# Optimization experiments

Hardware: AMD Instinct MI355X
Metric: run time of the kernel (lower is better)

Reference implementation:

```python
import jax, jax.numpy as jnp
import numpy as np

N_ANCHORS = 10647
N_CLASSES = 80
N_OUT = 5 + N_CLASSES
N_GT = 2048
POS_IOU = 0.7
NEG_IOU = 0.3
N_SAMPLE = 256
POS_RATIO = 0.5


def _cxcy_to_corners(b):
    return jnp.concatenate([b[:, :2] - b[:, 2:4] / 2, b[:, :2] + b[:, 2:4] / 2], axis=-1)


def _iou(a, b):
    # a: [N,4] corner boxes, b: [M,4] corner boxes -> [N,M]
    lt = jnp.maximum(a[:, None, :2], b[None, :, :2])
    rb = jnp.minimum(a[:, None, 2:], b[None, :, 2:])
    wh = jnp.clip(rb - lt, 0.0)
    inter = wh[..., 0] * wh[..., 1]
    area_a = (a[:, 2] - a[:, 0]) * (a[:, 3] - a[:, 1])
    area_b = (b[:, 2] - b[:, 0]) * (b[:, 3] - b[:, 1])
    return inter / (area_a[:, None] + area_b[None, :] - inter)


def _bce_logits(x, t):
    # numerically stable BCEWithLogits, elementwise
    return jnp.maximum(x, 0.0) - x * t + jnp.log1p(jnp.exp(-jnp.abs(x)))


def _demote_first(labels, value, excess):
    # demote the first `excess` anchors (in index order) whose label == value to -1,
    # mirroring torch's nonzero()[randperm(excess)] which always hits the first
    # `excess` entries of the nonzero list
    m = labels == value
    cum = jnp.cumsum(m.astype(jnp.int32))
    return jnp.where(m & (cum <= excess), -1.0, labels)


def _generate_targets(priors, gt_boxes, gt_labels):
    ious = _iou(_cxcy_to_corners(priors[:, :4]), _cxcy_to_corners(gt_boxes))  # [N, M]
    gt_max_index = jnp.argmax(ious, axis=0)       # [M] best anchor per gt
    anchor_max_ious = jnp.max(ious, axis=1)       # [N]
    anchor_max_index = jnp.argmax(ious, axis=1)   # [N]
    labels = jnp.full((N_ANCHORS,), -1.0, dtype=ious.dtype)
    labels = labels.at[gt_max_index].set(1.0)
    labels = jnp.where(anchor_max_ious >= POS_IOU, 1.0, labels)
    labels = jnp.where(anchor_max_ious < NEG_IOU, 0.0, labels)
    n_pos_quota = int(POS_RATIO * N_SAMPLE)
    n_pos_actual = jnp.sum(labels == 1.0)
    labels = _demote_first(labels, 1.0, jnp.maximum(n_pos_actual - n_pos_quota, 0))
    n_neg_req = N_SAMPLE - jnp.sum(labels == 1.0)
    n_neg_actual = jnp.sum(labels == 0.0)
    labels = _demote_first(labels, 0.0, jnp.maximum(n_neg_actual - n_neg_req, 0))
    anchor_gt_box = gt_boxes[anchor_max_index]    # [N,4] matched gt box per anchor
    anchor_cls = gt_labels[anchor_max_index] + 5  # [N] one-hot class column per anchor
    targets = jnp.zeros((N_ANCHORS, N_OUT), dtype=gt_boxes.dtype)
    targets = targets.at[:, :4].set(anchor_gt_box)
    targets = targets.at[:, 4].set(labels)
    targets = targets.at[jnp.arange(N_ANCHORS), anchor_cls].set(1.0)
    return targets


def _forward(predictions, gt_boxes, gt_labels, priors):
    targets = _generate_targets(priors, gt_boxes, gt_labels)
    pred = predictions[0]                          # [N, N_OUT]
    labels = targets[:, 4]
    pos = (labels == 1.0).astype(pred.dtype)
    neg = (labels == 0.0).astype(pred.dtype)
    n_pos = jnp.maximum(jnp.sum(pos), 1.0)
    n_neg = jnp.maximum(jnp.sum(neg), 1.0)
    # masked-mean MSE over x,y,w,h on positive anchors
    diff2 = (pred[:, :4] - targets[:, :4]) ** 2
    loss_box = jnp.sum(pos[:, None] * diff2, axis=0) / n_pos
    loss_conf_obj = jnp.sum(pos * _bce_logits(pred[:, 4], targets[:, 4])) / n_pos
    loss_conf_nonobj = jnp.sum(neg * _bce_logits(pred[:, 4], targets[:, 4])) / n_neg
    loss_class = jnp.sum(pos[:, None] * _bce_logits(pred[:, 5:], targets[:, 5:])) / (n_pos * N_CLASSES)
    total_loss = jnp.sum(loss_box) + loss_conf_obj + loss_conf_nonobj + loss_class
    return pred, total_loss


def setup_inputs() -> dict:
    key = jax.random.key(0)
    k1, k2, k3, k4 = jax.random.split(key, 4)
    predictions = jax.random.normal(k1, (1, N_ANCHORS, N_OUT), dtype=jnp.float32)
    gt_boxes = jax.random.uniform(k2, (N_GT, 4), dtype=jnp.float32, minval=0.05, maxval=0.95)
    gt_labels = jax.random.randint(k3, (N_GT,), 0, N_CLASSES)
    priors = jax.random.uniform(k4, (N_ANCHORS, N_OUT), dtype=jnp.float32, minval=0.05, maxval=0.95)
    return {"predictions": predictions, "gt_boxes": gt_boxes, "gt_labels": gt_labels, "priors": priors}


def reference(predictions, gt_boxes, gt_labels, priors):
    return _forward(predictions, gt_boxes, gt_labels, priors)
```

## Files before the change

kernel.cpp:

```cpp
#include <hip/hip_runtime.h>
#include <math.h>

#define N_ANCH 10647
#define N_GT   2048
#define N_OUTC 85
#define PRED_ELEMS (N_ANCH * N_OUTC)
#define PRED_V4    (PRED_ELEMS / 4)
#define N_CHUNK    42
#define NBMW       333

#define ABX 21
#define ABY 32
#define NBLK_A (ABX * ABY)
#define GBX 4
#define GBY 167
#define NBLK_G (GBX * GBY)
#define NBLK_IOU (NBLK_A + NBLK_G)
#define CPY_PER_BLK ((PRED_V4 + NBLK_IOU - 1) / NBLK_IOU)

struct WS {
    unsigned long long akey[N_ANCH];
    unsigned long long gkey[N_GT];
};
#define MEMSET_BYTES ((N_ANCH + N_GT) * 8)

__device__ __forceinline__ float bce(float x, float t) {
    return fmaxf(x, 0.0f) - x * t + log1pf(expf(-fabsf(x)));
}

__device__ __forceinline__ unsigned long long packkey(float iou, int idx) {
    return ((unsigned long long)__float_as_uint(iou) << 32) |
           (unsigned)(~(unsigned)idx);
}

__global__ __launch_bounds__(256) void k_iou(const float* __restrict__ pred,
                                             const float* __restrict__ gtb,
                                             const float* __restrict__ priors,
                                             float* __restrict__ out,
                                             WS* __restrict__ ws) {
    int b = blockIdx.x, t = threadIdx.x;
    if (t < CPY_PER_BLK) {
        int idx = b * CPY_PER_BLK + t;
        if (idx < PRED_V4)
            ((float4*)out)[idx] = ((const float4*)pred)[idx];
    }
    if (b == 0 && t == 0) {
        out[PRED_ELEMS - 3] = pred[PRED_ELEMS - 3];
        out[PRED_ELEMS - 2] = pred[PRED_ELEMS - 2];
        out[PRED_ELEMS - 1] = pred[PRED_ELEMS - 1];
        out[PRED_ELEMS] = 0.0f;
    }

    __shared__ float4 sc[64];
    __shared__ float  sa[64];

    if (b < NBLK_A) {
        int bx = b % ABX, by = b / ABX;
        int jbase = by * 64;
        if (t < 64) {
            float4 v = ((const float4*)gtb)[jbase + t];
            float4 c = make_float4(v.x - v.z*0.5f, v.y - v.w*0.5f,
                                   v.x + v.z*0.5f, v.y + v.w*0.5f);
            sc[t] = c;
            sa[t] = (c.z - c.x) * (c.w - c.y);
        }
        int i0 = bx * 512 + t, i1 = i0 + 256;
        bool v0 = (i0 < N_ANCH), v1 = (i1 < N_ANCH);
        float4 a0 = make_float4(0.f,0.f,0.f,0.f), a1 = a0;
        float aa0 = 0.f, aa1 = 0.f;
        if (v0) {
            float cx = priors[i0*N_OUTC+0], cy = priors[i0*N_OUTC+1];
            float w  = priors[i0*N_OUTC+2], h  = priors[i0*N_OUTC+3];
            a0 = make_float4(cx - w*0.5f, cy - h*0.5f, cx + w*0.5f, cy + h*0.5f);
            aa0 = (a0.z - a0.x) * (a0.w - a0.y);
        }
        if (v1) {
            float cx = priors[i1*N_OUTC+0], cy = priors[i1*N_OUTC+1];
            float w  = priors[i1*N_OUTC+2], h  = priors[i1*N_OUTC+3];
            a1 = make_float4(cx - w*0.5f, cy - h*0.5f, cx + w*0.5f, cy + h*0.5f);
            aa1 = (a1.z - a1.x) * (a1.w - a1.y);
        }
        __syncthreads();
        float I0 = -1.f, S0 = 1.f, I1 = -1.f, S1 = 1.f;
        int bj0 = 0, bj1 = 0;
#pragma unroll 4
        for (int jj = 0; jj < 64; ++jj) {
            float4 g = sc[jj]; float ga = sa[jj];
            float lx = fmaxf(a0.x, g.x), ly = fmaxf(a0.y, g.y);
            float rx = fminf(a0.z, g.z), ry = fminf(a0.w, g.w);
            float In = fmaxf(rx - lx, 0.f) * fmaxf(ry - ly, 0.f);
            float Sn = aa0 + ga;
            bool c = In * S0 > I0 * Sn;
            I0 = c ? In : I0; S0 = c ? Sn : S0; bj0 = c ? jj : bj0;
            lx = fmaxf(a1.x, g.x); ly = fmaxf(a1.y, g.y);
            rx = fminf(a1.z, g.z); ry = fminf(a1.w, g.w);
            In = fmaxf(rx - lx, 0.f) * fmaxf(ry - ly, 0.f);
            Sn = aa1 + ga;
            c = In * S1 > I1 * Sn;
            I1 = c ? In : I1; S1 = c ? Sn : S1; bj1 = c ? jj : bj1;
        }
        if (v0) atomicMax(&ws->akey[i0], packkey(I0 / (S0 - I0), jbase + bj0));
        if (v1) atomicMax(&ws->akey[i1], packkey(I1 / (S1 - I1), jbase + bj1));
    } else {
        int b2 = b - NBLK_A;
        int bx = b2 % GBX, by = b2 / GBX;
        int ibase = by * 64;
        if (t < 64) {
            int i = ibase + t;
            float4 c = make_float4(0.f, 0.f, 0.f, 0.f);
            float ar = 0.f;
            if (i < N_ANCH) {
                float cx = priors[i*N_OUTC+0], cy = priors[i*N_OUTC+1];
                float w  = priors[i*N_OUTC+2], h  = priors[i*N_OUTC+3];
                c = make_float4(cx - w*0.5f, cy - h*0.5f, cx + w*0.5f, cy + h*0.5f);
                ar = (c.z - c.x) * (c.w - c.y);
            }
            sc[t] = c; sa[t] = ar;
        }
        int j0 = bx * 512 + t, j1 = j0 + 256;
        float4 v = ((const float4*)gtb)[j0];
        float4 g0 = make_float4(v.x - v.z*0.5f, v.y - v.w*0.5f,
                                v.x + v.z*0.5f, v.y + v.w*0.5f);
        float ga0 = (g0.z - g0.x) * (g0.w - g0.y);
        v = ((const float4*)gtb)[j1];
        float4 g1 = make_float4(v.x - v.z*0.5f, v.y - v.w*0.5f,
                                v.x + v.z*0.5f, v.y + v.w*0.5f);
        float ga1 = (g1.z - g1.x) * (g1.w - g1.y);
        __syncthreads();
        float I0 = -1.f, S0 = 1.f, I1 = -1.f, S1 = 1.f;
        int bi0 = 0, bi1 = 0;
#pragma unroll 4
        for (int ii = 0; ii < 64; ++ii) {
            float4 a = sc[ii]; float aa = sa[ii];
            float lx = fmaxf(a.x, g0.x), ly = fmaxf(a.y, g0.y);
            float rx = fminf(a.z, g0.z), ry = fminf(a.w, g0.w);
            float In = fmaxf(rx - lx, 0.f) * fmaxf(ry - ly, 0.f);
            float Sn = aa + ga0;
            bool c = In * S0 > I0 * Sn;
            I0 = c ? In : I0; S0 = c ? Sn : S0; bi0 = c ? ii : bi0;
            lx = fmaxf(a.x, g1.x); ly = fmaxf(a.y, g1.y);
            rx = fminf(a.z, g1.z); ry = fminf(a.w, g1.w);
            In = fmaxf(rx - lx, 0.f) * fmaxf(ry - ly, 0.f);
            Sn = aa + ga1;
            c = In * S1 > I1 * Sn;
            I1 = c ? In : I1; S1 = c ? Sn : S1; bi1 = c ? ii : bi1;
        }
        atomicMax(&ws->gkey[j0], packkey(I0 / (S0 - I0), ibase + bi0));
        atomicMax(&ws->gkey[j1], packkey(I1 / (S1 - I1), ibase + bi1));
    }
}

__global__ __launch_bounds__(256) void k_tail(const float* __restrict__ pred,
                                              const float* __restrict__ gtb,
                                              const int* __restrict__ gtl,
                                              WS* __restrict__ ws,
                                              float* __restrict__ out) {
    __shared__ unsigned fbm[NBMW];
    __shared__ int wA[4], wB[4], wC[4], wD[4];
    __shared__ int wps[4], wns[4];
    __shared__ int    sPosI[256];
    __shared__ float4 sPosBox[256];
    __shared__ int    sPosCls[256];
    __shared__ int    sNegI[256];
    __shared__ float  red[12];
    int b = blockIdx.x, t = threadIdx.x, lane = t & 63, wid = t >> 6;

    for (int k = t; k < NBMW; k += 256) fbm[k] = 0u;
    __syncthreads();
    for (int j = t; j < N_GT; j += 256) {
        unsigned ai = ~(unsigned)(ws->gkey[j]);
        atomicOr(&fbm[ai >> 5], 1u << (ai & 31));
    }
    __syncthreads();

    const unsigned* akhi = ((const unsigned*)ws->akey) + 1;
    int npaW = 0, nnaW = 0, pbW = 0, nbW = 0;
    for (int c = 0; c < N_CHUNK; ++c) {
        int i = c * 256 + t;
        int lab = -2;
        if (i < N_ANCH) {
            float amax = __uint_as_float(akhi[2 * i]);
            bool fl = (fbm[i >> 5] >> (i & 31)) & 1u;
            lab = (amax < 0.3f) ? 0 : ((amax >= 0.7f || fl) ? 1 : -1);
        }
        int c1 = __popcll(__ballot(lab == 1));
        int c0 = __popcll(__ballot(lab == 0));
        npaW += c1; nnaW += c0;
        if (c < b) { pbW += c1; nbW += c0; }
    }
    if (lane == 0) { wA[wid] = npaW; wB[wid] = nnaW; wC[wid] = pbW; wD[wid] = nbW; }
    __syncthreads();
    int npa = wA[0]+wA[1]+wA[2]+wA[3];
    int nna = wB[0]+wB[1]+wB[2]+wB[3];
    int pb  = wC[0]+wC[1]+wC[2]+wC[3];
    int nb  = wD[0]+wD[1]+wD[2]+wD[3];

    int excess_pos = (npa > 128) ? (npa - 128) : 0;
    int n_pos_f = npa - excess_pos;
    int n_neg_req = 256 - n_pos_f;
    int excess_neg = (nna > n_neg_req) ? (nna - n_neg_req) : 0;
    int n_neg_f = nna - excess_neg;

    int i = b * 256 + t;
    int lab = -2;
    if (i < N_ANCH) {
        float amax = __uint_as_float(akhi[2 * i]);
        bool fl = (fbm[i >> 5] >> (i & 31)) & 1u;
        lab = (amax < 0.3f) ? 0 : ((amax >= 0.7f || fl) ? 1 : -1);
    }
    bool f1 = (lab == 1), f0 = (lab == 0);
    unsigned long long b1 = __ballot(f1), b0v = __ballot(f0);
    unsigned long long pm = (2ull << lane) - 1ull;
    int r1 = __popcll(b1 & pm), r0 = __popcll(b0v & pm);
    if (lane == 0) { wps[wid] = __popcll(b1); wns[wid] = __popcll(b0v); }
    __syncthreads();
    int p1 = 0, p0 = 0, cpB = 0, cnB = 0;
    for (int w = 0; w < 4; ++w) {
        int v1 = wps[w], v0 = wns[w];
        cpB += v1; cnB += v0;
        if (w < wid) { p1 += v1; p0 += v0; }
    }
    int thp = excess_pos - pb; thp = (thp < 0) ? 0 : thp;
    int thn = excess_neg - nb; thn = (thn < 0) ? 0 : thn;
    if (f1) {
        int L = p1 + r1;
        if (L > thp) {
            int slot = L - thp - 1;
            sPosI[slot] = i;
            unsigned am = ~(unsigned)(ws->akey[i]);
            sPosBox[slot] = ((const float4*)gtb)[am];
            sPosCls[slot] = gtl[am] + 5;
        }
    }
    if (f0) {
        int L = p0 + r0;
        if (L > thn) sNegI[L - thn - 1] = i;
    }
    __syncthreads();
    int nP = cpB - thp; nP = (nP < 0) ? 0 : nP;
    int nN = cnB - thn; nN = (nN < 0) ? 0 : nN;

    float acc_a = 0.f, acc_c = 0.f, acc_n = 0.f;
    int nT = nP * N_OUTC;
    for (int u = t; u < nT; u += 256) {
        int pi = u / N_OUTC, col = u - pi * N_OUTC;
        float p = pred[sPosI[pi] * N_OUTC + col];
        if (col < 4) {
            float d = p - ((const float*)&sPosBox[pi])[col];
            acc_a += d * d;
        } else if (col == 4) {
            acc_a += bce(p, 1.0f);
        } else {
            acc_c += bce(p, (col == sPosCls[pi]) ? 1.0f : 0.0f);
        }
    }
    for (int u = t; u < nN; u += 256)
        acc_n += bce(pred[sNegI[u] * N_OUTC + 4], 0.0f);

    for (int o = 32; o; o >>= 1) {
        acc_a += __shfl_down(acc_a, o);
        acc_c += __shfl_down(acc_c, o);
        acc_n += __shfl_down(acc_n, o);
    }
    if (lane == 0) { red[wid] = acc_a; red[4 + wid] = acc_c; red[8 + wid] = acc_n; }
    __syncthreads();
    if (t == 0) {
        float A  = red[0] + red[1] + red[2]  + red[3];
        float C  = red[4] + red[5] + red[6]  + red[7];
        float Nn = red[8] + red[9] + red[10] + red[11];
        float np = fmaxf((float)n_pos_f, 1.0f);
        float nn = fmaxf((float)n_neg_f, 1.0f);
        float contrib = A / np + Nn / nn + C / (np * 80.0f);
        if (contrib != 0.0f) atomicAdd(&out[PRED_ELEMS], contrib);
    }
}

extern "C" void kernel_launch(void* const* d_in, const int* in_sizes, int n_in,
                              void* d_out, int out_size, void* d_ws, size_t ws_size,
                              hipStream_t stream) {
    const float* pred   = (const float*)d_in[0];
    const float* gtb    = (const float*)d_in[1];
    const int*   gtl    = (const int*)d_in[2];
    const float* priors = (const float*)d_in[3];
    float* out = (float*)d_out;
    WS* ws = (WS*)d_ws;

    hipMemsetAsync(d_ws, 0, MEMSET_BYTES, stream);
    k_iou<<<dim3(NBLK_IOU), 256, 0, stream>>>(pred, gtb, priors, out, ws);
    k_tail<<<dim3(N_CHUNK), 256, 0, stream>>>(pred, gtb, gtl, ws, out);
}
```

Baseline: 77.65 us.

## Replace redundant per-block label recount with grid-wide atomic count exchange

Each tail block previously recomputed labels for all 42 chunks to get global and prefix positive/negative counts. Now each block computes labels only for its own 256 anchors, publishes its counts to workspace, and spin-waits on an atomic counter until all 42 blocks have published, then sums the counts from shared memory. This drops 42x redundant akey reads and the ballot loop, in exchange for a grid-wide spin barrier that relies on all 42 blocks being co-resident.

```diff
diff --git a/kernel.cpp b/kernel.cpp
--- a/kernel.cpp
+++ b/kernel.cpp
@@ -7,7 +7,6 @@
 #define PRED_ELEMS (N_ANCH * N_OUTC)
 #define PRED_V4    (PRED_ELEMS / 4)
 #define N_CHUNK    42
-#define NBMW       333
 
 #define ABX 21
 #define ABY 32
@@ -21,8 +20,9 @@
 struct WS {
     unsigned long long akey[N_ANCH];
     unsigned long long gkey[N_GT];
+    int cnt_p[N_CHUNK], cnt_n[N_CHUNK];
+    unsigned int sync;
 };
-#define MEMSET_BYTES ((N_ANCH + N_GT) * 8)
 
 __device__ __forceinline__ float bce(float x, float t) {
     return fmaxf(x, 0.0f) - x * t + log1pf(expf(-fabsf(x)));
@@ -150,66 +150,70 @@
     }
 }
 
-__global__ __launch_bounds__(256) void k_tail(const float* __restrict__ pred,
-                                              const float* __restrict__ gtb,
-                                              const int* __restrict__ gtl,
-                                              WS* __restrict__ ws,
-                                              float* __restrict__ out) {
-    __shared__ unsigned fbm[NBMW];
-    __shared__ int wA[4], wB[4], wC[4], wD[4];
+__global__ __launch_bounds__(256) void k_tail2(const float* __restrict__ pred,
+                                               const float* __restrict__ gtb,
+                                               const int* __restrict__ gtl,
+                                               WS* __restrict__ ws,
+                                               float* __restrict__ out) {
+    __shared__ int sFlg[256];
+    __shared__ int wA[4], wB[4];
     __shared__ int wps[4], wns[4];
+    __shared__ int sCp[N_CHUNK], sCn[N_CHUNK];
     __shared__ int    sPosI[256];
     __shared__ float4 sPosBox[256];
     __shared__ int    sPosCls[256];
     __shared__ int    sNegI[256];
     __shared__ float  red[12];
     int b = blockIdx.x, t = threadIdx.x, lane = t & 63, wid = t >> 6;
-
-    for (int k = t; k < NBMW; k += 256) fbm[k] = 0u;
+    int base = b * 256;
+
+    sFlg[t] = 0;
     __syncthreads();
     for (int j = t; j < N_GT; j += 256) {
-        unsigned ai = ~(unsigned)(ws->gkey[j]);
-        atomicOr(&fbm[ai >> 5], 1u << (ai & 31));
-    }
-    __syncthreads();
-
-    const unsigned* akhi = ((const unsigned*)ws->akey) + 1;
-    int npaW = 0, nnaW = 0, pbW = 0, nbW = 0;
+        int ai = (int)(~(unsigned)(ws->gkey[j]));
+        int rel = ai - base;
+        if ((unsigned)rel < 256u) sFlg[rel] = 1;
+    }
+    __syncthreads();
+    int i = base + t;
+    int lab = -2;
+    if (i < N_ANCH) {
+        float amax = __uint_as_float((unsigned)(ws->akey[i] >> 32));
+        lab = (amax < 0.3f) ? 0 : ((amax >= 0.7f || sFlg[t]) ? 1 : -1);
+    }
+    bool f1 = (lab == 1), f0 = (lab == 0);
+    unsigned long long b1 = __ballot(f1), b0v = __ballot(f0);
+    if (lane == 0) { wA[wid] = __popcll(b1); wB[wid] = __popcll(b0v); }
+    __syncthreads();
+    if (t == 0) {
+        int cp = wA[0] + wA[1] + wA[2] + wA[3];
+        int cn = wB[0] + wB[1] + wB[2] + wB[3];
+        __hip_atomic_store(&ws->cnt_p[b], cp, __ATOMIC_RELAXED, __HIP_MEMORY_SCOPE_AGENT);
+        __hip_atomic_store(&ws->cnt_n[b], cn, __ATOMIC_RELAXED, __HIP_MEMORY_SCOPE_AGENT);
+        __hip_atomic_fetch_add(&ws->sync, 1u, __ATOMIC_RELEASE, __HIP_MEMORY_SCOPE_AGENT);
+        while (__hip_atomic_load(&ws->sync, __ATOMIC_ACQUIRE, __HIP_MEMORY_SCOPE_AGENT)
+               < (unsigned)N_CHUNK)
+            __builtin_amdgcn_s_sleep(2);
+    }
+    __syncthreads();
+    if (t < N_CHUNK) {
+        sCp[t] = __hip_atomic_load(&ws->cnt_p[t], __ATOMIC_ACQUIRE, __HIP_MEMORY_SCOPE_AGENT);
+        sCn[t] = __hip_atomic_load(&ws->cnt_n[t], __ATOMIC_ACQUIRE, __HIP_MEMORY_SCOPE_AGENT);
+    }
+    __syncthreads();
+    int npa = 0, nna = 0, pb = 0, nb = 0;
+#pragma unroll
     for (int c = 0; c < N_CHUNK; ++c) {
-        int i = c * 256 + t;
-        int lab = -2;
-        if (i < N_ANCH) {
-            float amax = __uint_as_float(akhi[2 * i]);
-            bool fl = (fbm[i >> 5] >> (i & 31)) & 1u;
-            lab = (amax < 0.3f) ? 0 : ((amax >= 0.7f || fl) ? 1 : -1);
-        }
-        int c1 = __popcll(__ballot(lab == 1));
-        int c0 = __popcll(__ballot(lab == 0));
-        npaW += c1; nnaW += c0;
-        if (c < b) { pbW += c1; nbW += c0; }
-    }
-    if (lane == 0) { wA[wid] = npaW; wB[wid] = nnaW; wC[wid] = pbW; wD[wid] = nbW; }
-    __syncthreads();
-    int npa = wA[0]+wA[1]+wA[2]+wA[3];
-    int nna = wB[0]+wB[1]+wB[2]+wB[3];
-    int pb  = wC[0]+wC[1]+wC[2]+wC[3];
-    int nb  = wD[0]+wD[1]+wD[2]+wD[3];
-
+        int cp = sCp[c], cn = sCn[c];
+        if (c < b) { pb += cp; nb += cn; }
+        npa += cp; nna += cn;
+    }
     int excess_pos = (npa > 128) ? (npa - 128) : 0;
     int n_pos_f = npa - excess_pos;
     int n_neg_req = 256 - n_pos_f;
     int excess_neg = (nna > n_neg_req) ? (nna - n_neg_req) : 0;
     int n_neg_f = nna - excess_neg;
 
-    int i = b * 256 + t;
-    int lab = -2;
-    if (i < N_ANCH) {
-        float amax = __uint_as_float(akhi[2 * i]);
-        bool fl = (fbm[i >> 5] >> (i & 31)) & 1u;
-        lab = (amax < 0.3f) ? 0 : ((amax >= 0.7f || fl) ? 1 : -1);
-    }
-    bool f1 = (lab == 1), f0 = (lab == 0);
-    unsigned long long b1 = __ballot(f1), b0v = __ballot(f0);
     unsigned long long pm = (2ull << lane) - 1ull;
     int r1 = __popcll(b1 & pm), r0 = __popcll(b0v & pm);
     if (lane == 0) { wps[wid] = __popcll(b1); wns[wid] = __popcll(b0v); }
@@ -285,7 +289,7 @@
     float* out = (float*)d_out;
     WS* ws = (WS*)d_ws;
 
-    hipMemsetAsync(d_ws, 0, MEMSET_BYTES, stream);
+    hipMemsetAsync(d_ws, 0, sizeof(WS), stream);
     k_iou<<<dim3(NBLK_IOU), 256, 0, stream>>>(pred, gtb, priors, out, ws);
-    k_tail<<<dim3(N_CHUNK), 256, 0, stream>>>(pred, gtb, gtl, ws, out);
-}
+    k_tail2<<<dim3(N_CHUNK), 256, 0, stream>>>(pred, gtb, gtl, ws, out);
+}
```

New measurement: 66.42 us. 1.17x faster.
